# Kernel tuning notes

Measured on AMD Instinct MI355X. Metric: run time of the kernel, lower is better.

## Reference

```python
import jax, jax.numpy as jnp
import numpy as np
from jax import lax

# dims
B, S, NF, E = 128, 256, 32, 4
D, H = 256, 4
DI = 2 * D            # mLSTM inner (up-projection) dim
DHM, DHS = DI // H, D // H
K = 4                 # causal conv kernel size
FF = 352              # gated FFN dim (~4/3 * D, sLSTM block post-FFN)
NE, NP = 100, 6


def _ln(x, g, b, eps=1e-5):
    mu = x.mean(-1, keepdims=True)
    v = x.var(-1, keepdims=True)
    return (x - mu) / jnp.sqrt(v + eps) * g + b


def _cconv(x, w, b):
    # depthwise causal conv1d: x [B,S,C], w [K,C], b [C]
    k = w.shape[0]
    xp = jnp.pad(x, ((0, 0), (k - 1, 0), (0, 0)))
    y = lax.conv_general_dilated(xp, w[:, None, :], (1,), 'VALID',
                                 dimension_numbers=('NWC', 'WIO', 'NWC'),
                                 feature_group_count=x.shape[-1])
    return y + b


def _headnorm(x, g, b, eps=1e-6):
    # per-head group norm: normalize over last (head-dim) axis
    mu = x.mean(-1, keepdims=True)
    v = x.var(-1, keepdims=True)
    return (x - mu) / jnp.sqrt(v + eps) * g + b


def _forward(emb_esn, emb_prof, W_in, b_in,
             m_ln_g, m_ln_b, m_Wup, m_bup, m_convW, m_convb,
             m_Wq, m_bq, m_Wk, m_bk, m_Wv, m_bv,
             m_Wi, m_bi, m_Wf, m_bf, m_skip, m_ng, m_nb, m_Wdown, m_bdown,
             s_ln_g, s_ln_b, s_convW, s_convb,
             s_Wi, s_bi, s_Wf, s_bf, s_Wz, s_bz, s_Wo, s_bo,
             s_Ri, s_Rf, s_Rz, s_Ro, s_ng, s_nb,
             f_ln_g, f_ln_b, f_Wup, f_bup, f_Wdown, f_bdown,
             h_W1, h_b1, h_W2, h_b2,
             x_sens, x_esn, x_prof):
    Bx, Sx = x_sens.shape[0], x_sens.shape[1]
    ve = jnp.broadcast_to(emb_esn[x_esn][:, None, :], (Bx, Sx, E))
    vp = jnp.broadcast_to(emb_prof[x_prof][:, None, :], (Bx, Sx, E))
    x = jnp.concatenate([x_sens, ve, vp], -1) @ W_in + b_in  # [B,S,D]

    # ---------------- block 0: mLSTM (parallel stabilized matrix memory) ----
    xn = _ln(x, m_ln_g, m_ln_b)
    up = xn @ m_Wup + m_bup
    xm, zg = jnp.split(up, 2, axis=-1)              # [B,S,DI] each
    a = jax.nn.silu(_cconv(xm, m_convW, m_convb))   # causal conv + SiLU
    q = a @ m_Wq + m_bq
    k = a @ m_Wk + m_bk
    v = xm @ m_Wv + m_bv
    gin = jnp.concatenate([q, k, v], -1)            # [B,S,3*DI]
    ipre = (gin @ m_Wi + m_bi).transpose(0, 2, 1)   # [B,H,S]
    fpre = (gin @ m_Wf + m_bf).transpose(0, 2, 1)

    def heads(t, dh):
        return t.reshape(Bx, Sx, H, dh).transpose(0, 2, 1, 3)
    qh, kh, vh = heads(q, DHM), heads(k, DHM), heads(v, DHM)  # [B,H,S,dh]

    lfg = jax.nn.log_sigmoid(fpre)
    F = jnp.cumsum(lfg, -1)                         # [B,H,S]
    logD = F[:, :, :, None] - F[:, :, None, :] + ipre[:, :, None, :]
    mask = jnp.tril(jnp.ones((Sx, Sx), bool))
    logD = jnp.where(mask, logD, -jnp.inf)
    mstab = logD.max(-1, keepdims=True)             # [B,H,S,1]
    Dm = jnp.exp(logD - mstab)
    scores = jnp.einsum('bhtd,bhsd->bhts', qh, kh) / np.sqrt(DHM).astype(np.float32)
    C = scores * Dm
    nrm = jnp.maximum(jnp.abs(C.sum(-1, keepdims=True)), jnp.exp(-mstab))
    hh = jnp.einsum('bhts,bhsd->bhtd', C, vh) / nrm
    hn = _headnorm(hh, m_ng.reshape(1, H, 1, DHM), m_nb.reshape(1, H, 1, DHM))
    hn = hn.transpose(0, 2, 1, 3).reshape(Bx, Sx, DI)
    hn = hn + m_skip * a                            # learnable skip from conv branch
    x = x + (hn * jax.nn.silu(zg)) @ m_Wdown + m_bdown

    # ---------------- block 1: sLSTM (stabilized scalar recurrent scan) -----
    xn = _ln(x, s_ln_g, s_ln_b)
    ac = jax.nn.silu(_cconv(xn, s_convW, s_convb))
    to_t = lambda t: t.reshape(Bx, Sx, H, DHS).transpose(1, 0, 2, 3)  # [S,B,H,dh]
    it = to_t(ac @ s_Wi + s_bi)
    ft = to_t(ac @ s_Wf + s_bf)
    zt = to_t(xn @ s_Wz + s_bz)
    ot = to_t(xn @ s_Wo + s_bo)

    def step(carry, xs):
        h, c, n, m = carry
        i0, f0, z0, o0 = xs
        ip = i0 + jnp.einsum('bhd,hde->bhe', h, s_Ri)
        fp = f0 + jnp.einsum('bhd,hde->bhe', h, s_Rf)
        zp = jnp.tanh(z0 + jnp.einsum('bhd,hde->bhe', h, s_Rz))
        op = jax.nn.sigmoid(o0 + jnp.einsum('bhd,hde->bhe', h, s_Ro))
        mn = jnp.maximum(fp + m, ip)
        ig = jnp.exp(ip - mn)
        fg = jnp.exp(fp + m - mn)
        c = fg * c + ig * zp
        n = fg * n + ig
        h = op * c / n
        return (h, c, n, mn), h

    init = tuple(jnp.zeros((Bx, H, DHS), x.dtype) for _ in range(4))
    _, hs = lax.scan(step, init, (it, ft, zt, ot))  # hs [S,B,H,dh]
    hs = _headnorm(hs, s_ng.reshape(1, 1, H, DHS), s_nb.reshape(1, 1, H, DHS))
    x = x + hs.transpose(1, 0, 2, 3).reshape(Bx, Sx, D)

    # gated FFN (sLSTM block post-feedforward)
    xn = _ln(x, f_ln_g, f_ln_b)
    g_, u_ = jnp.split(xn @ f_Wup + f_bup, 2, axis=-1)
    x = x + (jax.nn.gelu(g_) * u_) @ f_Wdown + f_bdown

    last = x[:, -1, :]
    return jax.nn.relu(last @ h_W1 + h_b1) @ h_W2 + h_b2


def setup_inputs() -> dict:
    key = jax.random.key(0)
    ks = iter(jax.random.split(key, 64))
    nrm = lambda sh, s=0.02: jax.random.normal(next(ks), sh, jnp.float32) * s
    z = lambda sh: jnp.zeros(sh, jnp.float32)
    o = lambda sh: jnp.ones(sh, jnp.float32)
    return dict(
        x_sens=jax.random.normal(next(ks), (B, S, NF), jnp.float32),
        x_esn=jax.random.randint(next(ks), (B,), 0, NE, jnp.int32),
        x_prof=jax.random.randint(next(ks), (B,), 0, NP, jnp.int32),
        emb_esn=nrm((NE + 1, E)), emb_prof=nrm((NP + 1, E)),
        W_in=nrm((NF + 2 * E, D)), b_in=z((D,)),
        m_ln_g=o((D,)), m_ln_b=z((D,)),
        m_Wup=nrm((D, 2 * DI)), m_bup=z((2 * DI,)),
        m_convW=nrm((K, DI)), m_convb=z((DI,)),
        m_Wq=nrm((DI, DI)), m_bq=z((DI,)),
        m_Wk=nrm((DI, DI)), m_bk=z((DI,)),
        m_Wv=nrm((DI, DI)), m_bv=z((DI,)),
        m_Wi=nrm((3 * DI, H)), m_bi=z((H,)),
        m_Wf=nrm((3 * DI, H)), m_bf=o((H,)),
        m_skip=o((DI,)), m_ng=o((DI,)), m_nb=z((DI,)),
        m_Wdown=nrm((DI, D)), m_bdown=z((D,)),
        s_ln_g=o((D,)), s_ln_b=z((D,)),
        s_convW=nrm((K, D)), s_convb=z((D,)),
        s_Wi=nrm((D, D)), s_bi=z((D,)),
        s_Wf=nrm((D, D)), s_bf=o((D,)),
        s_Wz=nrm((D, D)), s_bz=z((D,)),
        s_Wo=nrm((D, D)), s_bo=z((D,)),
        s_Ri=nrm((H, DHS, DHS)), s_Rf=nrm((H, DHS, DHS)),
        s_Rz=nrm((H, DHS, DHS)), s_Ro=nrm((H, DHS, DHS)),
        s_ng=o((D,)), s_nb=z((D,)),
        f_ln_g=o((D,)), f_ln_b=z((D,)),
        f_Wup=nrm((D, 2 * FF)), f_bup=z((2 * FF,)),
        f_Wdown=nrm((FF, D)), f_bdown=z((D,)),
        h_W1=nrm((D, 64), 0.05), h_b1=z((64,)),
        h_W2=nrm((64, 3), 0.05), h_b2=z((3,)),
    )


def reference(emb_esn, emb_prof, W_in, b_in,
              m_ln_g, m_ln_b, m_Wup, m_bup, m_convW, m_convb,
              m_Wq, m_bq, m_Wk, m_bk, m_Wv, m_bv,
              m_Wi, m_bi, m_Wf, m_bf, m_skip, m_ng, m_nb, m_Wdown, m_bdown,
              s_ln_g, s_ln_b, s_convW, s_convb,
              s_Wi, s_bi, s_Wf, s_bf, s_Wz, s_bz, s_Wo, s_bo,
              s_Ri, s_Rf, s_Rz, s_Ro, s_ng, s_nb,
              f_ln_g, f_ln_b, f_Wup, f_bup, f_Wdown, f_bdown,
              h_W1, h_b1, h_W2, h_b2,
              x_sens, x_esn, x_prof):
    return _forward(emb_esn, emb_prof, W_in, b_in,
                    m_ln_g, m_ln_b, m_Wup, m_bup, m_convW, m_convb,
                    m_Wq, m_bq, m_Wk, m_bk, m_Wv, m_bv,
                    m_Wi, m_bi, m_Wf, m_bf, m_skip, m_ng, m_nb, m_Wdown, m_bdown,
                    s_ln_g, s_ln_b, s_convW, s_convb,
                    s_Wi, s_bi, s_Wf, s_bf, s_Wz, s_bz, s_Wo, s_bo,
                    s_Ri, s_Rf, s_Rz, s_Ro, s_ng, s_nb,
                    f_ln_g, f_ln_b, f_Wup, f_bup, f_Wdown, f_bdown,
                    h_W1, h_b1, h_W2, h_b2,
                    x_sens, x_esn, x_prof)
```

## Files before the change

### kernel.cpp

```cpp
#include <hip/hip_runtime.h>
#include <cstdint>
#include <cstddef>


using u16 = unsigned short;
using u32 = unsigned int;

typedef __attribute__((ext_vector_type(8))) short short8;
typedef __attribute__((ext_vector_type(8))) unsigned short ushort8v;
typedef __attribute__((ext_vector_type(4))) float float4v;

#define DEVINL __device__ __forceinline__

DEVINL float b2f(u16 u){ u32 x = ((u32)u) << 16; return __builtin_bit_cast(float, x); }
DEVINL u16 f2b(float f){
  u32 x = __builtin_bit_cast(u32, f);
  u32 r = x + 0x7FFFu + ((x >> 16) & 1u);
  return (u16)(r >> 16);
}
DEVINL float ldval(float x){ return x; }
DEVINL float ldval(u16 x){ return b2f(x); }
DEVINL void stval(float* p, float v){ *p = v; }
DEVINL void stval(u16* p, float v){ *p = f2b(v); }

DEVINL void dpp_sum2(float a, float b, float& oa, float& ob){
  int xa, xb;
  xa = __builtin_amdgcn_update_dpp(0, __builtin_bit_cast(int, a), 0x111, 0xf, 0xf, true);
  xb = __builtin_amdgcn_update_dpp(0, __builtin_bit_cast(int, b), 0x111, 0xf, 0xf, true);
  a += __builtin_bit_cast(float, xa); b += __builtin_bit_cast(float, xb);
  xa = __builtin_amdgcn_update_dpp(0, __builtin_bit_cast(int, a), 0x112, 0xf, 0xf, true);
  xb = __builtin_amdgcn_update_dpp(0, __builtin_bit_cast(int, b), 0x112, 0xf, 0xf, true);
  a += __builtin_bit_cast(float, xa); b += __builtin_bit_cast(float, xb);
  xa = __builtin_amdgcn_update_dpp(0, __builtin_bit_cast(int, a), 0x114, 0xf, 0xf, true);
  xb = __builtin_amdgcn_update_dpp(0, __builtin_bit_cast(int, b), 0x114, 0xf, 0xf, true);
  a += __builtin_bit_cast(float, xa); b += __builtin_bit_cast(float, xb);
  xa = __builtin_amdgcn_update_dpp(0, __builtin_bit_cast(int, a), 0x118, 0xf, 0xf, true);
  xb = __builtin_amdgcn_update_dpp(0, __builtin_bit_cast(int, b), 0x118, 0xf, 0xf, true);
  a += __builtin_bit_cast(float, xa); b += __builtin_bit_cast(float, xb);
  xa = __builtin_amdgcn_update_dpp(0, __builtin_bit_cast(int, a), 0x142, 0xf, 0xf, true);
  xb = __builtin_amdgcn_update_dpp(0, __builtin_bit_cast(int, b), 0x142, 0xf, 0xf, true);
  a += __builtin_bit_cast(float, xa); b += __builtin_bit_cast(float, xb);
  xa = __builtin_amdgcn_update_dpp(0, __builtin_bit_cast(int, a), 0x143, 0xf, 0xf, true);
  xb = __builtin_amdgcn_update_dpp(0, __builtin_bit_cast(int, b), 0x143, 0xf, 0xf, true);
  a += __builtin_bit_cast(float, xa); b += __builtin_bit_cast(float, xb);
  oa = __builtin_bit_cast(float, __builtin_amdgcn_readlane(__builtin_bit_cast(int, a), 63));
  ob = __builtin_bit_cast(float, __builtin_amdgcn_readlane(__builtin_bit_cast(int, b), 63));
}

constexpr int IN_N = 56;
constexpr long long IN_SIZES[IN_N] = {
  1048576, 128, 128, 404, 28, 10240, 256, 256, 256,
  262144, 1024, 2048, 512,
  262144, 512, 262144, 512, 262144, 512,
  6144, 4, 6144, 4,
  512, 512, 512, 131072, 256,
  256, 256, 1024, 256,
  65536, 256, 65536, 256, 65536, 256, 65536, 256,
  16384, 16384, 16384, 16384,
  256, 256,
  256, 256, 180224, 704, 90112, 256,
  16384, 64, 192, 3 };

constexpr bool is_wt_input(int i){
  return i==9 || i==13 || i==15 || i==17 || i==26 || i==32 || i==34 || i==36
      || i==38 || i==48 || i==50;
}

struct CvOff { long long off[IN_N+1]; };
constexpr CvOff make_off(){
  CvOff o{};
  long long a = 0;
  for (int i = 0; i < IN_N; i++){
    o.off[i] = a;
    long long s = IN_SIZES[i];
    if (i == 1 || i == 2 || is_wt_input(i)) s = 0;
    a += s;
  }
  o.off[IN_N] = a;
  return o;
}
constexpr CvOff CVOFF = make_off();
constexpr long long CV_TOTAL = CVOFF.off[IN_N];

constexpr int WT_NW = 11;
constexpr int WTB_IN[WT_NW] = {9, 13, 15, 17, 26, 32, 34, 36, 38, 48, 50};
constexpr int WTB_K[WT_NW]  = {256,512,512,512,512,256,256,256,256,256,352};
constexpr int WTB_N[WT_NW]  = {1024,512,512,512,256,256,256,256,256,704,256};
constexpr long long WTO[WT_NW+1] = {0, 262144, 524288, 786432, 1048576, 1179648,
  1245184, 1310720, 1376256, 1441792, 1622016, 1712128};
constexpr long long WT_ELEMS = WTO[WT_NW];

constexpr long long alignup(long long x){ return ((x + 255) / 256) * 256; }
constexpr long long TOK = 32768;
constexpr long long OFF_FLAG = alignup(CV_TOTAL);
constexpr long long OFF_IP  = OFF_FLAG + 64;
constexpr long long OFF_FP  = OFF_IP  + 131072;
constexpr long long OFF_F   = OFF_FP  + 131072;
constexpr long long OFF_G   = OFF_F   + 131072;
constexpr long long OFF_M   = OFF_G   + 131072;
constexpr long long OFF_X   = OFF_M   + 131072;
constexpr long long OFF_XN  = OFF_X   + TOK*256;
constexpr long long OFF_UP  = OFF_XN  + TOK*128;
constexpr long long OFF_A   = OFF_UP  + TOK*512;
constexpr long long OFF_Q   = OFF_A   + TOK*256;
constexpr long long OFF_K   = OFF_Q   + TOK*256;
constexpr long long OFF_V   = OFF_K   + TOK*256;
constexpr long long OFF_WT  = OFF_V   + TOK*256;
constexpr long long WS_END  = OFF_WT  + WT_ELEMS/2 + 256;


__global__ void detect_kernel(const void* mlng, int* flag){
  if (threadIdx.x == 0){
    u32 u = *(const u32*)mlng;
    *flag = (u == 0x3F803F80u) ? 1 : 0;
  }
}

struct InPtrs { const void* p[IN_N]; };

__global__ __launch_bounds__(256) void convert_kernel(InPtrs ptrs, float* __restrict__ cv,
                                                      const int* __restrict__ flag){
  long long gid = (long long)blockIdx.x * 256 + threadIdx.x;
  if (gid >= CV_TOTAL) return;
  int seg = 0;
#pragma unroll
  for (int i = 1; i < IN_N; i++) seg += (gid >= CVOFF.off[i]) ? 1 : 0;
  long long local = gid - CVOFF.off[seg];
  float v;
  if (*flag) v = b2f(((const u16*)ptrs.p[seg])[local]);
  else       v = ((const float*)ptrs.p[seg])[local];
  cv[gid] = v;
}

__global__ __launch_bounds__(256) void wtrans_kernel(InPtrs ptrs, u16* __restrict__ WTb,
                                                     const int* __restrict__ flag){
  int wz = blockIdx.z;
  int K = WTB_K[wz], N = WTB_N[wz];
  int n0 = blockIdx.x * 32, k0 = blockIdx.y * 32;
  if (n0 >= N || k0 >= K) return;
  const void* W = ptrs.p[WTB_IN[wz]];
  u16* WT = WTb + WTO[wz];
  __shared__ u16 tile[32][34];
  int tx = threadIdx.x & 31, ty = threadIdx.x >> 5;
  bool bf = (*flag != 0);
#pragma unroll
  for (int i = 0; i < 4; i++){
    size_t src = (size_t)(k0 + ty + i*8)*N + n0 + tx;
    tile[ty + i*8][tx] = bf ? ((const u16*)W)[src] : f2b(((const float*)W)[src]);
  }
  __syncthreads();
#pragma unroll
  for (int i = 0; i < 4; i++)
    WT[(size_t)(n0 + ty + i*8)*K + k0 + tx] = tile[tx][ty + i*8];
}

__global__ __launch_bounds__(256) void cat_kernel(const float* __restrict__ xs,
    const int* __restrict__ xe, const int* __restrict__ xp,
    const float* __restrict__ ee, const float* __restrict__ ep,
    float* __restrict__ CAT){
  int gid = blockIdx.x * 256 + threadIdx.x;
  int c = gid % 40; int t = gid / 40; int b = t >> 8;
  float v;
  if (c < 32)      v = xs[(size_t)t*32 + c];
  else if (c < 36) v = ee[xe[b]*4 + (c - 32)];
  else             v = ep[xp[b]*4 + (c - 36)];
  CAT[(size_t)t*40 + c] = v;
}

template<typename TA, typename TC>
__global__ __launch_bounds__(256) void gemm_kernel(
    const TA* __restrict__ A, int lda,
    const float* __restrict__ Wm, const float* __restrict__ bias,
    TC* __restrict__ Cc, int ldc, const float* __restrict__ resid,
    int M, int N, int K)
{
  __shared__ float As[16][68];
  __shared__ float Bs[16][68];
  const int bm = blockIdx.y * 64, bn = blockIdx.x * 64;
  const int tid = threadIdx.x, tx = tid & 15, ty = tid >> 4;
  float acc[4][4] = {};
  for (int k0 = 0; k0 < K; k0 += 16){
#pragma unroll
    for (int i = 0; i < 4; i++){
      int idx = tid + i*256;
      int m = idx >> 4, kq = idx & 15;
      As[kq][m] = (k0 + kq < K) ? ldval(A[(size_t)(bm + m)*lda + k0 + kq]) : 0.f;
      int kk = idx >> 6, n = idx & 63;
      Bs[kk][n] = (k0 + kk < K) ? Wm[(size_t)(k0 + kk)*N + bn + n] : 0.f;
    }
    __syncthreads();
#pragma unroll
    for (int kq = 0; kq < 16; kq++){
      float av[4], bv[4];
#pragma unroll
      for (int i = 0; i < 4; i++) av[i] = As[kq][ty*4 + i];
#pragma unroll
      for (int j = 0; j < 4; j++) bv[j] = Bs[kq][tx*4 + j];
#pragma unroll
      for (int i = 0; i < 4; i++)
#pragma unroll
        for (int j = 0; j < 4; j++) acc[i][j] += av[i]*bv[j];
    }
    __syncthreads();
  }
#pragma unroll
  for (int i = 0; i < 4; i++){
    int m = bm + ty*4 + i;
#pragma unroll
    for (int j = 0; j < 4; j++){
      int n = bn + tx*4 + j;
      float v = acc[i][j] + bias[n];
      if (resid) v += resid[(size_t)m*ldc + n];
      stval(&Cc[(size_t)m*ldc + n], v);
    }
  }
}

template<typename TC>
__global__ __launch_bounds__(256) void gemm_mfma(
    const u16* __restrict__ A, int lda,
    const u16* __restrict__ WT,
    const float* __restrict__ bias,
    TC* __restrict__ Cc, int ldc, const float* __restrict__ resid,
    int N, int K)
{
  __shared__ alignas(16) u16 As[2][128*40];
  __shared__ alignas(16) u16 Bs[2][128*40];
  const int bm = blockIdx.y * 128, bn = blockIdx.x * 128;
  const int tid = threadIdx.x;
  const int w = tid >> 6, lane = tid & 63, lm = lane & 15, q = lane >> 4;
  const int wm = w >> 1, wn = w & 1;
  const int r0c = tid >> 2, ch0 = tid & 3;
  const int r1c = (tid + 256) >> 2, ch1 = tid & 3;
  float4v acc[4][4] = {};

  {
    *(uint4*)&As[0][r0c*40 + ch0*8] = *(const uint4*)&A[(size_t)(bm + r0c)*lda + ch0*8];
    int n0 = bn + r0c;
    uint4 bv0 = {0u,0u,0u,0u};
    if (n0 < N) bv0 = *(const uint4*)&WT[(size_t)n0*K + ch0*8];
    *(uint4*)&Bs[0][r0c*40 + ch0*8] = bv0;
    *(uint4*)&As[0][r1c*40 + ch1*8] = *(const uint4*)&A[(size_t)(bm + r1c)*lda + ch1*8];
    int n1 = bn + r1c;
    uint4 bv1 = {0u,0u,0u,0u};
    if (n1 < N) bv1 = *(const uint4*)&WT[(size_t)n1*K + ch1*8];
    *(uint4*)&Bs[0][r1c*40 + ch1*8] = bv1;
  }
  __syncthreads();
  int cur = 0;
  for (int k0 = 32; k0 < K; k0 += 32){
    uint4 av0 = *(const uint4*)&A[(size_t)(bm + r0c)*lda + k0 + ch0*8];
    uint4 av1 = *(const uint4*)&A[(size_t)(bm + r1c)*lda + k0 + ch1*8];
    int n0 = bn + r0c, n1 = bn + r1c;
    uint4 bv0 = {0u,0u,0u,0u}, bv1 = {0u,0u,0u,0u};
    if (n0 < N) bv0 = *(const uint4*)&WT[(size_t)n0*K + k0 + ch0*8];
    if (n1 < N) bv1 = *(const uint4*)&WT[(size_t)n1*K + k0 + ch1*8];
    short8 a[4], b[4];
#pragma unroll
    for (int i = 0; i < 4; i++)
      a[i] = *(const short8*)&As[cur][(wm*64 + i*16 + lm)*40 + q*8];
#pragma unroll
    for (int j = 0; j < 4; j++)
      b[j] = *(const short8*)&Bs[cur][(wn*64 + j*16 + lm)*40 + q*8];
#pragma unroll
    for (int i = 0; i < 4; i++)
#pragma unroll
      for (int j = 0; j < 4; j++)
        acc[i][j] = __builtin_amdgcn_mfma_f32_16x16x32_bf16(a[i], b[j], acc[i][j], 0, 0, 0);
    *(uint4*)&As[cur^1][r0c*40 + ch0*8] = av0;
    *(uint4*)&Bs[cur^1][r0c*40 + ch0*8] = bv0;
    *(uint4*)&As[cur^1][r1c*40 + ch1*8] = av1;
    *(uint4*)&Bs[cur^1][r1c*40 + ch1*8] = bv1;
    __syncthreads();
    cur ^= 1;
  }
  {
    short8 a[4], b[4];
#pragma unroll
    for (int i = 0; i < 4; i++)
      a[i] = *(const short8*)&As[cur][(wm*64 + i*16 + lm)*40 + q*8];
#pragma unroll
    for (int j = 0; j < 4; j++)
      b[j] = *(const short8*)&Bs[cur][(wn*64 + j*16 + lm)*40 + q*8];
#pragma unroll
    for (int i = 0; i < 4; i++)
#pragma unroll
      for (int j = 0; j < 4; j++)
        acc[i][j] = __builtin_amdgcn_mfma_f32_16x16x32_bf16(a[i], b[j], acc[i][j], 0, 0, 0);
  }
#pragma unroll
  for (int i = 0; i < 4; i++){
#pragma unroll
    for (int j = 0; j < 4; j++){
      int col = bn + wn*64 + j*16 + lm;
      if (col < N){
#pragma unroll
        for (int r = 0; r < 4; r++){
          int row = bm + wm*64 + i*16 + q*4 + r;
          float v = acc[i][j][r] + bias[col];
          if (resid) v += resid[(size_t)row*ldc + col];
          stval(&Cc[(size_t)row*ldc + col], v);
        }
      }
    }
  }
}

__global__ __launch_bounds__(256) void ln_kernel(const float* __restrict__ Xin,
    const float* __restrict__ g, const float* __restrict__ b,
    u16* __restrict__ out, float eps){
  int t = blockIdx.x*4 + (threadIdx.x >> 6);
  int e = threadIdx.x & 63;
  float4 v = *(const float4*)&Xin[(size_t)t*256 + e*4];
  float su = v.x + v.y + v.z + v.w;
#pragma unroll
  for (int o = 32; o > 0; o >>= 1) su += __shfl_xor(su, o, 64);
  float mu = su * (1.f/256.f);
  float d0 = v.x - mu, d1 = v.y - mu, d2 = v.z - mu, d3 = v.w - mu;
  float sq = d0*d0 + d1*d1 + d2*d2 + d3*d3;
#pragma unroll
  for (int o = 32; o > 0; o >>= 1) sq += __shfl_xor(sq, o, 64);
  float rstd = rsqrtf(sq * (1.f/256.f) + eps);
  float4 gv = *(const float4*)&g[e*4];
  float4 bv = *(const float4*)&b[e*4];
  ushort4 o4;
  o4.x = f2b(d0*rstd*gv.x + bv.x);
  o4.y = f2b(d1*rstd*gv.y + bv.y);
  o4.z = f2b(d2*rstd*gv.z + bv.z);
  o4.w = f2b(d3*rstd*gv.w + bv.w);
  *(ushort4*)&out[(size_t)t*256 + e*4] = o4;
}

__global__ __launch_bounds__(256) void conv_silu_kernel(const u16* __restrict__ Xc, int ldx, int C,
    const float* __restrict__ w, const float* __restrict__ bias, u16* __restrict__ Y){
  int nc = C >> 3;
  long long gid = (long long)blockIdx.x * 256 + threadIdx.x;
  int c8 = (int)(gid % nc) * 8; long long t = gid / nc;
  int s = (int)(t & 255);
  float acc[8];
#pragma unroll
  for (int i = 0; i < 8; i++) acc[i] = bias[c8 + i];
#pragma unroll
  for (int j = 0; j < 4; j++){
    int so = s - 3 + j;
    if (so >= 0){
      ushort8v xv = *(const ushort8v*)&Xc[(size_t)(t - 3 + j)*ldx + c8];
#pragma unroll
      for (int i = 0; i < 8; i++) acc[i] += b2f(xv[i]) * w[j*C + c8 + i];
    }
  }
  ushort8v o8;
#pragma unroll
  for (int i = 0; i < 8; i++) o8[i] = f2b(acc[i] / (1.f + __expf(-acc[i])));
  *(ushort8v*)&Y[(size_t)t*C + c8] = o8;
}

__global__ __launch_bounds__(256) void gates_kernel(
    const u16* __restrict__ Q, const u16* __restrict__ Kb, const u16* __restrict__ V,
    const float* __restrict__ Wi, const float* __restrict__ bi,
    const float* __restrict__ Wf, const float* __restrict__ bf,
    float* __restrict__ IP, float* __restrict__ FP){
  int t = blockIdx.x; int tid = threadIdx.x;
  int o = tid & 7, seg = tid >> 3;
  int b = t >> 8, s = t & 255;
  int g = o & 3;
  const float* Wg = (o >= 4) ? Wf : Wi;
  float part = 0.f;
#pragma unroll
  for (int i = 0; i < 6; i++){
    int k8 = seg*48 + i*8;
    const u16* src; int off;
    if (k8 < 512){ src = Q; off = k8; }
    else if (k8 < 1024){ src = Kb; off = k8 - 512; }
    else { src = V; off = k8 - 1024; }
    ushort8v gv = *(const ushort8v*)&src[(size_t)t*512 + off];
#pragma unroll
    for (int j = 0; j < 8; j++) part += b2f(gv[j]) * Wg[(k8 + j)*4 + g];
  }
  __shared__ float red[256];
  red[tid] = part; __syncthreads();
  if (tid < 8){
    float tot = 0.f;
    for (int ss = 0; ss < 32; ss++) tot += red[ss*8 + tid];
    int gg = tid & 3;
    if (tid < 4) IP[(b*4 + gg)*256 + s] = tot + bi[gg];
    else         FP[(b*4 + gg)*256 + s] = tot + bf[gg];
  }
}

__global__ __launch_bounds__(256) void fscan_kernel(const float* __restrict__ IP,
    const float* __restrict__ FP, float* __restrict__ Fo, float* __restrict__ Go,
    float* __restrict__ Mo){
  int bh = blockIdx.x; int s = threadIdx.x;
  int idx = bh*256 + s;
  __shared__ float buf[256];
  float fp = FP[idx];
  float lfg = fminf(fp, 0.f) - log1pf(expf(-fabsf(fp)));
  float v = lfg;
  buf[s] = v; __syncthreads();
  for (int off = 1; off < 256; off <<= 1){
    float tv = (s >= off) ? buf[s - off] : 0.f;
    __syncthreads();
    v += tv; buf[s] = v;
    __syncthreads();
  }
  float Fv = v;
  float g = IP[idx] - Fv;
  float mv = g;
  buf[s] = mv; __syncthreads();
  for (int off = 1; off < 256; off <<= 1){
    float tv = (s >= off) ? buf[s - off] : -3.0e38f;
    __syncthreads();
    mv = fmaxf(mv, tv); buf[s] = mv;
    __syncthreads();
  }
  Fo[idx] = Fv; Go[idx] = g; Mo[idx] = mv;
}

__global__ __launch_bounds__(256) void attn_kernel(
    const u16* __restrict__ Q, const u16* __restrict__ Kb, const u16* __restrict__ V,
    const float* __restrict__ G, const float* __restrict__ Mx, const float* __restrict__ F,
    const u16* __restrict__ Ab, const u16* __restrict__ UPb,
    const float* __restrict__ ng, const float* __restrict__ nb,
    const float* __restrict__ skip, u16* __restrict__ Yb)
{
  int bh = blockIdx.y, b = bh >> 2, h = bh & 3;
  int tt = blockIdx.x, t0 = tt * 64;
  int tid = threadIdx.x;
  int w = tid >> 6, lane = tid & 63, lm = lane & 15, q = lane >> 4;
  int gbase = bh * 256;

  __shared__ alignas(16) u16 Qs[64*136];
  __shared__ alignas(16) u16 Ks[64*136];
  __shared__ alignas(16) u16 Vt[128*72];
  __shared__ alignas(16) u16 Ps[64*72];
  __shared__ float rs[64];

#pragma unroll
  for (int c = tid; c < 1024; c += 256){
    int r = c >> 4, ch = c & 15;
    *(uint4*)&Qs[r*136 + ch*8] =
      *(const uint4*)&Q[((size_t)(b*256 + t0 + r))*512 + h*128 + ch*8];
  }
  if (tid < 64) rs[tid] = 0.f;

  float mrow[4];
#pragma unroll
  for (int r = 0; r < 4; r++) mrow[r] = Mx[gbase + t0 + w*16 + q*4 + r];

  float4v acc2[8] = {};
  const float scale = 0.08838834764831845f;

  for (int ss = 0; ss <= tt; ss++){
    int s0 = ss * 64;
    __syncthreads();
#pragma unroll
    for (int c = tid; c < 1024; c += 256){
      int r = c >> 4, ch = c & 15;
      *(uint4*)&Ks[r*136 + ch*8] =
        *(const uint4*)&Kb[((size_t)(b*256 + s0 + r))*512 + h*128 + ch*8];
    }
#pragma unroll
    for (int c = tid; c < 1024; c += 256){
      int sl = c & 63, db = c >> 6;
      ushort8v v = *(const ushort8v*)&V[((size_t)(b*256 + s0 + sl))*512 + h*128 + db*8];
#pragma unroll
      for (int j = 0; j < 8; j++) Vt[(db*8 + j)*72 + sl] = v[j];
    }
    __syncthreads();
    float4v sacc[4] = {};
#pragma unroll
    for (int k0 = 0; k0 < 128; k0 += 32){
      short8 a = *(const short8*)&Qs[(w*16 + lm)*136 + k0 + q*8];
#pragma unroll
      for (int j = 0; j < 4; j++){
        short8 bb = *(const short8*)&Ks[(j*16 + lm)*136 + k0 + q*8];
        sacc[j] = __builtin_amdgcn_mfma_f32_16x16x32_bf16(a, bb, sacc[j], 0, 0, 0);
      }
    }
    float rp[4] = {0.f, 0.f, 0.f, 0.f};
#pragma unroll
    for (int j = 0; j < 4; j++){
      int scol = s0 + j*16 + lm;
      float gq = G[gbase + scol];
#pragma unroll
      for (int r = 0; r < 4; r++){
        int trow = t0 + w*16 + q*4 + r;
        float cval = (scol <= trow) ? sacc[j][r]*scale*__expf(gq - mrow[r]) : 0.f;
        Ps[(w*16 + q*4 + r)*72 + j*16 + lm] = f2b(cval);
        rp[r] += cval;
      }
    }
#pragma unroll
    for (int r = 0; r < 4; r++){
#pragma unroll
      for (int m = 1; m < 16; m <<= 1) rp[r] += __shfl_xor(rp[r], m, 16);
      if (lm == 0) rs[w*16 + q*4 + r] += rp[r];
    }
#pragma unroll
    for (int k0 = 0; k0 < 64; k0 += 32){
      short8 a = *(const short8*)&Ps[(w*16 + lm)*72 + k0 + q*8];
#pragma unroll
      for (int jd = 0; jd < 8; jd++){
        short8 bb = *(const short8*)&Vt[(jd*16 + lm)*72 + k0 + q*8];
        acc2[jd] = __builtin_amdgcn_mfma_f32_16x16x32_bf16(a, bb, acc2[jd], 0, 0, 0);
      }
    }
  }
  __syncthreads();
#pragma unroll
  for (int r = 0; r < 4; r++){
    int rl = w*16 + q*4 + r;
    int t = t0 + rl;
    float Fv = F[gbase + t];
    float nrm = fmaxf(fabsf(rs[rl]), __expf(-(Fv + mrow[r])));
    float inv = 1.f / nrm;
    float vv[8];
    float su = 0.f;
#pragma unroll
    for (int jd = 0; jd < 8; jd++){ vv[jd] = acc2[jd][r]*inv; su += vv[jd]; }
#pragma unroll
    for (int m = 1; m < 16; m <<= 1) su += __shfl_xor(su, m, 16);
    float mu = su * (1.f/128.f);
    float sq = 0.f;
#pragma unroll
    for (int jd = 0; jd < 8; jd++){ vv[jd] -= mu; sq += vv[jd]*vv[jd]; }
#pragma unroll
    for (int m = 1; m < 16; m <<= 1) sq += __shfl_xor(sq, m, 16);
    float rstd = rsqrtf(sq * (1.f/128.f) + 1e-6f);
#pragma unroll
    for (int jd = 0; jd < 8; jd++){
      int c = h*128 + jd*16 + lm;
      float hv = vv[jd]*rstd*ng[c] + nb[c];
      float av = b2f(Ab[(size_t)t*512 + c]);
      float zg = b2f(UPb[(size_t)t*1024 + 512 + c]);
      float sz = zg / (1.f + __expf(-zg));
      Yb[(size_t)t*512 + c] = f2b((hv + skip[c]*av)*sz);
    }
  }
}

__global__ __launch_bounds__(320) void scan_kernel(
    const float* __restrict__ G1, const float* __restrict__ G2,
    const float* __restrict__ Ri, const float* __restrict__ Rf,
    const float* __restrict__ Rz, const float* __restrict__ Ro,
    const float* __restrict__ sng, const float* __restrict__ snb,
    float* __restrict__ Xr){
  int bh = blockIdx.x; int b = bh >> 2, h = bh & 3;
  int e = threadIdx.x & 63;
  int w = threadIdx.x >> 6;
  __shared__ float4 part[2][4][64];
  __shared__ float hbuf[2][64];
  size_t xrow = ((size_t)b*256)*256 + h*64 + e;

  if (w < 4){
    float r0[16], r1[16], r2[16], r3[16];
    const float* Rp0 = Ri + h*4096 + w*1024;
    const float* Rp1 = Rf + h*4096 + w*1024;
    const float* Rp2 = Rz + h*4096 + w*1024;
    const float* Rp3 = Ro + h*4096 + w*1024;
#pragma unroll
    for (int d = 0; d < 16; d++){
      r0[d] = Rp0[d*64 + e];
      r1[d] = Rp1[d*64 + e];
      r2[d] = Rp2[d*64 + e];
      r3[d] = Rp3[d*64 + e];
    }
    const float* Gp = (w < 2) ? G1 : G2;
    size_t grow = ((size_t)b*256)*512 + ((w & 1) ? 256 : 0) + h*64 + e;
    float hS = 0.f, cS = 0.f, nS = 0.f, mS = 0.f;
    float gv = Gp[grow];
    float gn = Gp[grow + 512];
    for (int s = 0; s < 256; s++){
      float gn2 = 0.f;
      if (s < 254) gn2 = Gp[grow + (size_t)(s + 2)*512];
      float ai0 = 0.f, ai1 = 0.f, af0 = 0.f, af1 = 0.f;
      float az0 = 0.f, az1 = 0.f, ao0 = 0.f, ao1 = 0.f;
#pragma unroll
      for (int k = 0; k < 16; k += 2){
        float h0 = __builtin_bit_cast(float,
            __builtin_amdgcn_readlane(__builtin_bit_cast(int, hS), w*16 + k));
        float h1 = __builtin_bit_cast(float,
            __builtin_amdgcn_readlane(__builtin_bit_cast(int, hS), w*16 + k + 1));
        ai0 += h0*r0[k]; ai1 += h1*r0[k+1];
        af0 += h0*r1[k]; af1 += h1*r1[k+1];
        az0 += h0*r2[k]; az1 += h1*r2[k+1];
        ao0 += h0*r3[k]; ao1 += h1*r3[k+1];
      }
      float4 p;
      p.x = ai0 + ai1; p.y = af0 + af1; p.z = az0 + az1; p.w = ao0 + ao1;
      if      (w == 0) p.x += gv;
      else if (w == 1) p.y += gv;
      else if (w == 2) p.z += gv;
      else             p.w += gv;
      part[s & 1][w][e] = p;
      __syncthreads();
      float4 q0 = part[s & 1][0][e];
      float4 q1 = part[s & 1][1][e];
      float4 q2 = part[s & 1][2][e];
      float4 q3 = part[s & 1][3][e];
      float ip = (q0.x + q1.x) + (q2.x + q3.x);
      float fp = (q0.y + q1.y) + (q2.y + q3.y);
      float zr = (q0.z + q1.z) + (q2.z + q3.z);
      float og = (q0.w + q1.w) + (q2.w + q3.w);
      float zp = 1.f - 2.f*__builtin_amdgcn_rcpf(__expf(2.f*zr) + 1.f);
      float op = __builtin_amdgcn_rcpf(1.f + __expf(-og));
      float mn = fmaxf(fp + mS, ip);
      float ig = __expf(ip - mn);
      float fg = __expf(fp + mS - mn);
      cS = fg*cS + ig*zp;
      nS = fg*nS + ig;
      mS = mn;
      hS = op * cS * __builtin_amdgcn_rcpf(nS);
      if (w == 1) hbuf[s & 1][e] = hS;
      gv = gn; gn = gn2;
    }
    __syncthreads();
  } else {
    float gw = sng[h*64 + e], bw = snb[h*64 + e];
    float xp = 0.f, xc = 0.f;
    for (int s = 0; s < 256; s++){
      xc = Xr[xrow + (size_t)s*256];
      __syncthreads();
      if (s > 0){
        float hv = hbuf[(s - 1) & 1][e];
        float su, sq;
        dpp_sum2(hv, hv*hv, su, sq);
        float mu = su * (1.f/64.f);
        float var = fmaxf(sq * (1.f/64.f) - mu*mu, 0.f);
        float nv = (hv - mu) * rsqrtf(var + 1e-6f) * gw + bw;
        Xr[xrow + (size_t)(s - 1)*256] = xp + nv;
      }
      xp = xc;
    }
    __syncthreads();
    float hv = hbuf[1][e];
    float su, sq;
    dpp_sum2(hv, hv*hv, su, sq);
    float mu = su * (1.f/64.f);
    float var = fmaxf(sq * (1.f/64.f) - mu*mu, 0.f);
    float nv = (hv - mu) * rsqrtf(var + 1e-6f) * gw + bw;
    Xr[xrow + (size_t)255*256] = xp + nv;
  }
}

__global__ __launch_bounds__(256) void ffn_act_kernel(const u16* __restrict__ GU,
                                                      u16* __restrict__ P){
  long long gid = (long long)blockIdx.x * 256 + threadIdx.x;
  int j8 = (int)(gid % 44) * 8; long long t = gid / 44;
  ushort8v gv = *(const ushort8v*)&GU[(size_t)t*704 + j8];
  ushort8v uv = *(const ushort8v*)&GU[(size_t)t*704 + 352 + j8];
  ushort8v o8;
#pragma unroll
  for (int i = 0; i < 8; i++){
    float g = b2f(gv[i]);
    float u = b2f(uv[i]);
    float inner = 0.7978845608028654f * (g + 0.044715f*g*g*g);
    float gel = 0.5f * g * (1.f + tanhf(inner));
    o8[i] = f2b(gel * u);
  }
  *(ushort8v*)&P[(size_t)t*352 + j8] = o8;
}

__global__ __launch_bounds__(64) void head_kernel(const float* __restrict__ X,
    const float* __restrict__ W1, const float* __restrict__ b1,
    const float* __restrict__ W2, const float* __restrict__ b2,
    void* out, const int* __restrict__ flag){
  int b = blockIdx.x, j = threadIdx.x;
  __shared__ float L[256];
  __shared__ float H1[64];
  for (int i = j; i < 256; i += 64) L[i] = X[((size_t)(b*256 + 255))*256 + i];
  __syncthreads();
  float acc = b1[j];
  for (int d = 0; d < 256; d++) acc += L[d] * W1[d*64 + j];
  H1[j] = fmaxf(acc, 0.f);
  __syncthreads();
  if (j < 3){
    float o = b2[j];
    for (int k2 = 0; k2 < 64; k2++) o += H1[k2] * W2[k2*3 + j];
    if (*flag) ((u16*)out)[b*3 + j] = f2b(o);
    else       ((float*)out)[b*3 + j] = o;
  }
}

extern "C" void kernel_launch(void* const* d_in, const int* in_sizes, int n_in,
                              void* d_out, int out_size, void* d_ws, size_t ws_size,
                              hipStream_t stream)
{
  if (n_in != IN_N) return;
  for (int i = 0; i < IN_N; i++) if ((long long)in_sizes[i] != IN_SIZES[i]) return;
  if (ws_size < (size_t)WS_END * 4) return;
  if (out_size != 384) return;

  float* ws = (float*)d_ws;
  float* cv = ws;
  auto cvp = [&](int i){ return cv + CVOFF.off[i]; };

  int*   flag = (int*)(ws + OFF_FLAG);
  float* IP   = ws + OFF_IP;
  float* FP   = ws + OFF_FP;
  float* Fb   = ws + OFF_F;
  float* Gb   = ws + OFF_G;
  float* Mb   = ws + OFF_M;
  float* X    = ws + OFF_X;
  u16*   XNb  = (u16*)(ws + OFF_XN);
  u16*   UPb  = (u16*)(ws + OFF_UP);
  u16*   Ab   = (u16*)(ws + OFF_A);
  u16*   Qb   = (u16*)(ws + OFF_Q);
  u16*   Kbb  = (u16*)(ws + OFF_K);
  u16*   Vb   = (u16*)(ws + OFF_V);
  u16*   WTb  = (u16*)(ws + OFF_WT);
  float* CAT = ws + OFF_V;
  u16*   Yb  = Qb;
  u16*   ACb = Ab;
  float* G1f = ws + OFF_K;
  float* G2f = ws + OFF_UP;
  u16*   GUb = UPb;
  u16*   Pb  = Ab;

  auto wt = [&](int widx){ return WTb + WTO[widx]; };

  InPtrs ptrs;
  for (int i = 0; i < IN_N; i++) ptrs.p[i] = d_in[i];

  const int M = 32768;
  detect_kernel<<<1, 64, 0, stream>>>(d_in[7], flag);
  int cvblocks = (int)((CV_TOTAL + 255) / 256);
  convert_kernel<<<cvblocks, 256, 0, stream>>>(ptrs, cv, flag);
  wtrans_kernel<<<dim3(32, 16, 11), 256, 0, stream>>>(ptrs, WTb, flag);
  cat_kernel<<<5120, 256, 0, stream>>>(cvp(0), (const int*)d_in[1], (const int*)d_in[2],
                                       cvp(3), cvp(4), CAT);
  gemm_kernel<float, float><<<dim3(4, 512), 256, 0, stream>>>(CAT, 40, cvp(5), cvp(6),
      X, 256, nullptr, M, 256, 40);
  ln_kernel<<<8192, 256, 0, stream>>>(X, cvp(7), cvp(8), XNb, 1e-5f);
  gemm_mfma<u16><<<dim3(8, 256), 256, 0, stream>>>(XNb, 256, wt(0), cvp(10),
      UPb, 1024, nullptr, 1024, 256);
  conv_silu_kernel<<<8192, 256, 0, stream>>>(UPb, 1024, 512, cvp(11), cvp(12), Ab);
  gemm_mfma<u16><<<dim3(4, 256), 256, 0, stream>>>(Ab, 512, wt(1), cvp(14),
      Qb, 512, nullptr, 512, 512);
  gemm_mfma<u16><<<dim3(4, 256), 256, 0, stream>>>(Ab, 512, wt(2), cvp(16),
      Kbb, 512, nullptr, 512, 512);
  gemm_mfma<u16><<<dim3(4, 256), 256, 0, stream>>>(UPb, 1024, wt(3), cvp(18),
      Vb, 512, nullptr, 512, 512);
  gates_kernel<<<M, 256, 0, stream>>>(Qb, Kbb, Vb, cvp(19), cvp(20), cvp(21), cvp(22), IP, FP);
  fscan_kernel<<<512, 256, 0, stream>>>(IP, FP, Fb, Gb, Mb);
  attn_kernel<<<dim3(4, 512), 256, 0, stream>>>(Qb, Kbb, Vb, Gb, Mb, Fb,
      Ab, UPb, cvp(24), cvp(25), cvp(23), Yb);
  gemm_mfma<float><<<dim3(2, 256), 256, 0, stream>>>(Yb, 512, wt(4), cvp(27),
      X, 256, X, 256, 512);
  ln_kernel<<<8192, 256, 0, stream>>>(X, cvp(28), cvp(29), XNb, 1e-5f);
  conv_silu_kernel<<<4096, 256, 0, stream>>>(XNb, 256, 256, cvp(30), cvp(31), ACb);
  gemm_mfma<float><<<dim3(4, 256), 256, 0, stream>>>(ACb, 256, wt(5), cvp(33),
      G1f, 512, nullptr, 512, 256);
  gemm_mfma<float><<<dim3(4, 256), 256, 0, stream>>>(XNb, 256, wt(7), cvp(37),
      G2f, 512, nullptr, 512, 256);
  scan_kernel<<<512, 320, 0, stream>>>(G1f, G2f, cvp(40), cvp(41), cvp(42), cvp(43),
      cvp(44), cvp(45), X);
  ln_kernel<<<8192, 256, 0, stream>>>(X, cvp(46), cvp(47), XNb, 1e-5f);
  gemm_mfma<u16><<<dim3(6, 256), 256, 0, stream>>>(XNb, 256, wt(9), cvp(49),
      GUb, 704, nullptr, 704, 256);
  ffn_act_kernel<<<5632, 256, 0, stream>>>(GUb, Pb);
  gemm_mfma<float><<<dim3(2, 256), 256, 0, stream>>>(Pb, 352, wt(10), cvp(51),
      X, 256, X, 256, 352);
  head_kernel<<<128, 64, 0, stream>>>(X, cvp(52), cvp(53), cvp(54), cvp(55), d_out, flag);
}
```

Baseline: 1.063 ms.

## Load GEMM tiles directly into LDS with XOR-swizzled layout

Replaces the register-staged global-to-LDS copies in the MFMA GEMM with direct global_load_lds 16-byte transfers, and swaps the padded 40-element row stride for an unpadded 32-element stride with an XOR column swizzle to avoid bank conflicts. This removes the VGPR round trip and the ds_write instructions from the main loop and shrinks LDS use. The bounds check on N for the weight rows is dropped, so the code now assumes N is a multiple of 128, and correctness depends on the swizzle on the write side matching the one on the read side.

```diff
diff --git a/kernel.cpp b/kernel.cpp
--- a/kernel.cpp
+++ b/kernel.cpp
@@ -22,6 +22,12 @@
 DEVINL float ldval(u16 x){ return b2f(x); }
 DEVINL void stval(float* p, float v){ *p = v; }
 DEVINL void stval(u16* p, float v){ *p = f2b(v); }
+
+DEVINL void glds16(const void* g, void* l){
+  __builtin_amdgcn_global_load_lds(
+      (const __attribute__((address_space(1))) unsigned int*)g,
+      (__attribute__((address_space(3))) unsigned int*)l, 16, 0, 0);
+}
 
 DEVINL void dpp_sum2(float a, float b, float& oa, float& ob){
   int xa, xb;
@@ -224,53 +230,46 @@
     TC* __restrict__ Cc, int ldc, const float* __restrict__ resid,
     int N, int K)
 {
-  __shared__ alignas(16) u16 As[2][128*40];
-  __shared__ alignas(16) u16 Bs[2][128*40];
+  __shared__ alignas(16) u16 As[2][128*32];
+  __shared__ alignas(16) u16 Bs[2][128*32];
   const int bm = blockIdx.y * 128, bn = blockIdx.x * 128;
   const int tid = threadIdx.x;
   const int w = tid >> 6, lane = tid & 63, lm = lane & 15, q = lane >> 4;
   const int wm = w >> 1, wn = w & 1;
-  const int r0c = tid >> 2, ch0 = tid & 3;
-  const int r1c = (tid + 256) >> 2, ch1 = tid & 3;
+  const int rA0 = w*16 + (lane >> 2);
+  const int rA1 = 64 + rA0;
+  const int csw = (lane & 3) ^ ((lane >> 3) & 3);
+  const u16* aSrc0 = A  + (size_t)(bm + rA0)*lda + csw*8;
+  const u16* aSrc1 = A  + (size_t)(bm + rA1)*lda + csw*8;
+  const u16* bSrc0 = WT + (size_t)(bn + rA0)*K   + csw*8;
+  const u16* bSrc1 = WT + (size_t)(bn + rA1)*K   + csw*8;
+  const int cq = (lm >> 1) & 3;
+  const int rdA = (q ^ cq) << 3;
   float4v acc[4][4] = {};
 
-  {
-    *(uint4*)&As[0][r0c*40 + ch0*8] = *(const uint4*)&A[(size_t)(bm + r0c)*lda + ch0*8];
-    int n0 = bn + r0c;
-    uint4 bv0 = {0u,0u,0u,0u};
-    if (n0 < N) bv0 = *(const uint4*)&WT[(size_t)n0*K + ch0*8];
-    *(uint4*)&Bs[0][r0c*40 + ch0*8] = bv0;
-    *(uint4*)&As[0][r1c*40 + ch1*8] = *(const uint4*)&A[(size_t)(bm + r1c)*lda + ch1*8];
-    int n1 = bn + r1c;
-    uint4 bv1 = {0u,0u,0u,0u};
-    if (n1 < N) bv1 = *(const uint4*)&WT[(size_t)n1*K + ch1*8];
-    *(uint4*)&Bs[0][r1c*40 + ch1*8] = bv1;
-  }
+  glds16(aSrc0, &As[0][w*512]);
+  glds16(aSrc1, &As[0][2048 + w*512]);
+  glds16(bSrc0, &Bs[0][w*512]);
+  glds16(bSrc1, &Bs[0][2048 + w*512]);
   __syncthreads();
   int cur = 0;
   for (int k0 = 32; k0 < K; k0 += 32){
-    uint4 av0 = *(const uint4*)&A[(size_t)(bm + r0c)*lda + k0 + ch0*8];
-    uint4 av1 = *(const uint4*)&A[(size_t)(bm + r1c)*lda + k0 + ch1*8];
-    int n0 = bn + r0c, n1 = bn + r1c;
-    uint4 bv0 = {0u,0u,0u,0u}, bv1 = {0u,0u,0u,0u};
-    if (n0 < N) bv0 = *(const uint4*)&WT[(size_t)n0*K + k0 + ch0*8];
-    if (n1 < N) bv1 = *(const uint4*)&WT[(size_t)n1*K + k0 + ch1*8];
+    glds16(aSrc0 + k0, &As[cur^1][w*512]);
+    glds16(aSrc1 + k0, &As[cur^1][2048 + w*512]);
+    glds16(bSrc0 + k0, &Bs[cur^1][w*512]);
+    glds16(bSrc1 + k0, &Bs[cur^1][2048 + w*512]);
     short8 a[4], b[4];
 #pragma unroll
     for (int i = 0; i < 4; i++)
-      a[i] = *(const short8*)&As[cur][(wm*64 + i*16 + lm)*40 + q*8];
+      a[i] = *(const short8*)&As[cur][(wm*64 + i*16 + lm)*32 + rdA];
 #pragma unroll
     for (int j = 0; j < 4; j++)
-      b[j] = *(const short8*)&Bs[cur][(wn*64 + j*16 + lm)*40 + q*8];
+      b[j] = *(const short8*)&Bs[cur][(wn*64 + j*16 + lm)*32 + rdA];
 #pragma unroll
     for (int i = 0; i < 4; i++)
 #pragma unroll
       for (int j = 0; j < 4; j++)
         acc[i][j] = __builtin_amdgcn_mfma_f32_16x16x32_bf16(a[i], b[j], acc[i][j], 0, 0, 0);
-    *(uint4*)&As[cur^1][r0c*40 + ch0*8] = av0;
-    *(uint4*)&Bs[cur^1][r0c*40 + ch0*8] = bv0;
-    *(uint4*)&As[cur^1][r1c*40 + ch1*8] = av1;
-    *(uint4*)&Bs[cur^1][r1c*40 + ch1*8] = bv1;
     __syncthreads();
     cur ^= 1;
   }
@@ -278,10 +277,10 @@
     short8 a[4], b[4];
 #pragma unroll
     for (int i = 0; i < 4; i++)
-      a[i] = *(const short8*)&As[cur][(wm*64 + i*16 + lm)*40 + q*8];
+      a[i] = *(const short8*)&As[cur][(wm*64 + i*16 + lm)*32 + rdA];
 #pragma unroll
     for (int j = 0; j < 4; j++)
-      b[j] = *(const short8*)&Bs[cur][(wn*64 + j*16 + lm)*40 + q*8];
+      b[j] = *(const short8*)&Bs[cur][(wn*64 + j*16 + lm)*32 + rdA];
 #pragma unroll
     for (int i = 0; i < 4; i++)
 #pragma unroll
```

Measured after the change: 1.072 ms. No clear change (+0.9%).
